# Kernel tuning notes

Hardware: AMD Instinct MI355X
Metric: run time of the kernel (lower is better)

## Reference

```python
import jax, jax.numpy as jnp
import numpy as np

TAU = 2.0        # LIF membrane time constant
VTH = 1.0        # firing threshold
ALPHA = 4.0      # surrogate sigmoid sharpness
BN_EPS = 1e-5

@jax.custom_vjp
def heaviside_surrogate(x):
    # Forward: hard threshold. Backward: sigmoid surrogate gradient (alpha=4).
    return (x >= 0.0).astype(x.dtype)

def _hs_fwd(x):
    return heaviside_surrogate(x), x

def _hs_bwd(x, g):
    s = jax.nn.sigmoid(ALPHA * x)
    return (g * ALPHA * s * (1.0 - s),)

heaviside_surrogate.defvjp(_hs_fwd, _hs_bwd)


def setup_inputs() -> dict:
    key = jax.random.key(0)
    k1, k2 = jax.random.split(key)
    B, Cin, T, Cout = 64, 512, 1024, 256
    x = jax.random.normal(k1, (B, Cin, T), dtype=jnp.float32)
    W = jax.random.normal(k2, (Cout, Cin), dtype=jnp.float32) * (1.0 / np.sqrt(Cin))
    gamma = jnp.ones((Cout,), dtype=jnp.float32)
    beta = jnp.zeros((Cout,), dtype=jnp.float32)
    run_mean = jnp.zeros((Cout,), dtype=jnp.float32)
    run_var = jnp.ones((Cout,), dtype=jnp.float32)
    return {"x": x, "W": W, "gamma": gamma, "beta": beta,
            "run_mean": run_mean, "run_var": run_var}


def reference(x, W, gamma, beta, run_mean, run_var):
    # Dropout is identity in eval mode.
    # conv1d, kernel_size=1, no bias -> pointwise GEMM over channels: [B,Cin,T] -> [B,Cout,T]
    y = jnp.einsum('bct,oc->bot', x, W)
    # BatchNorm1d (inference, running stats), per-channel affine
    inv = jax.lax.rsqrt(run_var + BN_EPS)
    y = (y - run_mean[None, :, None]) * (inv * gamma)[None, :, None] + beta[None, :, None]
    # LIF recurrence over the time dim (last axis), hard reset to 0, detach_reset.
    yt = jnp.transpose(y, (2, 0, 1))  # [T, B, Cout]

    def step(v, x_t):
        v = v + (x_t - v) / TAU              # decay_input charge
        s = heaviside_surrogate(v - VTH)     # spike via surrogate threshold
        v = v * (1.0 - jax.lax.stop_gradient(s))  # hard reset (detached)
        return v, s

    v0 = jnp.zeros(yt.shape[1:], dtype=yt.dtype)
    _, spikes = jax.lax.scan(step, v0, yt)   # spikes: [T, B, Cout]
    # out.mean(dim=-1) == spike rate over time
    return spikes.mean(axis=0)               # [B, Cout]
```

## Files before the change

### kernel.cpp

```cpp
#include <hip/hip_runtime.h>
#include <math.h>

typedef _Float16 f16;
typedef __attribute__((ext_vector_type(8)))  _Float16 f16v8;
typedef __attribute__((ext_vector_type(4)))  __fp16   h16v4;
typedef __attribute__((ext_vector_type(16))) float    f32x16;
typedef __attribute__((ext_vector_type(4)))  float    f32x4;

namespace {
constexpr int kB = 64, kCin = 512, kT = 1024, kCout = 256;
constexpr size_t kYBytes     = (size_t)kB * kT * kCout * 4;
constexpr size_t kWfragBytes = (size_t)32 * 8 * 2 * 64 * 16;
constexpr size_t kSBytes     = kCout * 4;
constexpr size_t kWsNeed     = kYBytes + kWfragBytes + kSBytes;
}

__global__ void wsplit16_kernel(const float* __restrict__ W, const float* __restrict__ gamma,
                                const float* __restrict__ rvar,
                                f16* __restrict__ wfrag, float* __restrict__ sarr) {
    const int kc = blockIdx.x, osub = blockIdx.y, p = blockIdx.z;
    const int lane = threadIdx.x;
    const int o  = osub * 32 + (lane & 31);
    const int kb = kc * 16 + (lane >> 5) * 8;
    f16v8 frag;
#pragma unroll
    for (int j = 0; j < 8; ++j) {
        const float w = 32.0f * W[o * kCin + kb + j];
        const f16 h = (f16)w;
        const float r = w - (float)h;
        const f16 l = (f16)(r * 2048.0f);
        frag[j] = p ? l : h;
    }
    *reinterpret_cast<f16v8*>(wfrag + ((size_t)((kc * 8 + osub) * 2 + p) * 64 + lane) * 8) = frag;
    if (kc == 0 && osub == 0 && p == 0) {
#pragma unroll
        for (int j = 0; j < 4; ++j) {
            const int oo = j * 64 + lane;
            sarr[oo] = (float)((double)gamma[oo] / sqrt((double)rvar[oo] + 1e-5));
        }
    }
}

__global__ __launch_bounds__(512, 2)
void gemm_f16_kernel(const float* __restrict__ x, const f16* __restrict__ wfrag,
                     const float* __restrict__ sarr, const float* __restrict__ rmean,
                     const float* __restrict__ beta, float* __restrict__ yt) {
    __shared__ unsigned int Bd[4][128 * 20];

    const int tid  = threadIdx.x;
    const int lane = tid & 63;
    const int wave = tid >> 6;
    const int n = lane & 31, q = lane >> 5;

    const int bid  = blockIdx.x;
    const int rest = bid >> 3;
    const int b    = (bid & 7) + 8 * (rest >> 3);
    const int tg0  = (rest & 7) * 128;
    const int osg  = wave;
    const float* __restrict__ xb = x + ((size_t)b << 19);
    const f16v8* __restrict__ wf = reinterpret_cast<const f16v8*>(wfrag);

    const int st_t = tid & 127;
    const int kpp  = tid >> 7;
    const int st_sw = (st_t >> 3) & 3;
    const int wr_base = 20 * st_t + 2 * (kpp & 1);
    const int s0 = ((0 + (kpp >> 1)) ^ st_sw) * 4;
    const int s1 = ((2 + (kpp >> 1)) ^ st_sw) * 4;

    f32x16 accA[4] = {};
    f32x16 accB[4] = {};
    f16v8  af[2][2];
    float  xq[4][4];

    auto loadX = [&](int kc, float (&xd)[4]) {
        const float* px = xb + (size_t)(kc * 16 + 4 * kpp) * kT + tg0 + st_t;
#pragma unroll
        for (int r = 0; r < 4; ++r) xd[r] = px[(size_t)r * kT];
    };
    auto loadA = [&](int kc, f16v8 (&ad)[2]) {
#pragma unroll
        for (int pp = 0; pp < 2; ++pp)
            ad[pp] = wf[(size_t)((kc * 8 + osg) * 2 + pp) * 64 + lane];
    };
    auto stage = [&](int buf, const float (&xd)[4]) {
        auto h01 = __builtin_amdgcn_cvt_pkrtz(xd[0], xd[1]);
        auto h23 = __builtin_amdgcn_cvt_pkrtz(xd[2], xd[3]);
        auto l01 = __builtin_amdgcn_cvt_pkrtz((xd[0] - (float)h01[0]) * 2048.0f,
                                              (xd[1] - (float)h01[1]) * 2048.0f);
        auto l23 = __builtin_amdgcn_cvt_pkrtz((xd[2] - (float)h23[0]) * 2048.0f,
                                              (xd[3] - (float)h23[1]) * 2048.0f);
        h16v4 hv, lv;
        hv[0] = h01[0]; hv[1] = h01[1]; hv[2] = h23[0]; hv[3] = h23[1];
        lv[0] = l01[0]; lv[1] = l01[1]; lv[2] = l23[0]; lv[3] = l23[1];
        *reinterpret_cast<h16v4*>(&Bd[buf][wr_base + s0]) = hv;
        *reinterpret_cast<h16v4*>(&Bd[buf][wr_base + s1]) = lv;
    };
    auto domfma = [&](int buf, const f16v8 (&ad)[2]) {
        __builtin_amdgcn_s_setprio(1);
#pragma unroll
        for (int s = 0; s < 4; ++s) {
            const int t = s * 32 + n;
            const int sw = (t >> 3) & 3;
            const f16v8 bh = *reinterpret_cast<const f16v8*>(&Bd[buf][20 * t + 4 * ((0 + q) ^ sw)]);
            const f16v8 bl = *reinterpret_cast<const f16v8*>(&Bd[buf][20 * t + 4 * ((2 + q) ^ sw)]);
            accA[s] = __builtin_amdgcn_mfma_f32_32x32x16_f16(ad[0], bh, accA[s], 0, 0, 0);
            accB[s] = __builtin_amdgcn_mfma_f32_32x32x16_f16(ad[0], bl, accB[s], 0, 0, 0);
            accB[s] = __builtin_amdgcn_mfma_f32_32x32x16_f16(ad[1], bh, accB[s], 0, 0, 0);
        }
        __builtin_amdgcn_s_setprio(0);
    };

    loadX(0, xq[0]); loadX(1, xq[1]); loadX(2, xq[2]); loadX(3, xq[3]);
    loadA(0, af[0]);
    stage(0, xq[0]);
    stage(1, xq[1]);
    asm volatile("s_waitcnt lgkmcnt(0)\n\ts_barrier" ::: "memory");

    for (int kc4 = 0; kc4 < 8; ++kc4) {
#pragma unroll
        for (int u = 0; u < 4; ++u) {
            const int kc = kc4 * 4 + u;
            if (kc < 31) loadA(kc + 1, af[(u + 1) & 1]);
            if (kc < 30) stage((u + 2) & 3, xq[(u + 2) & 3]);
            if (kc < 28) loadX(kc + 4, xq[u]);
            domfma(u, af[u & 1]);
            if (u & 1)
                asm volatile("s_waitcnt lgkmcnt(0)\n\ts_barrier" ::: "memory");
        }
    }

#pragma unroll
    for (int s = 0; s < 4; ++s) {
        const f32x16 v = accA[s] + accB[s] * 4.8828125e-4f;
        const size_t t = (size_t)tg0 + s * 32 + n;
#pragma unroll
        for (int g = 0; g < 4; ++g) {
            const int og = osg * 32 + g * 8 + q * 4;
            const f32x4 sv = *reinterpret_cast<const f32x4*>(sarr + og);
            const f32x4 mv = *reinterpret_cast<const f32x4*>(rmean + og);
            const f32x4 bv = *reinterpret_cast<const f32x4*>(beta + og);
#pragma unroll
            for (int r2 = 0; r2 < 4; ++r2) {
                const int o = og + r2;
                const float val = (v[4 * g + r2] * 0.03125f - mv[r2]) * sv[r2] + bv[r2];
                yt[(((size_t)b << 8) + (size_t)o) * 1024 + t] = val;
            }
        }
    }
}

__global__ __launch_bounds__(64)
void lif_kernel(const float* __restrict__ yt, float* __restrict__ out) {
    const int b = blockIdx.x >> 2;
    const int o = ((blockIdx.x & 3) << 6) + threadIdx.x;
    const f32x4* __restrict__ row =
        reinterpret_cast<const f32x4*>(yt) + (((size_t)b << 8) + (size_t)o) * 256;
    float v = 0.f;
    int cnt = 0;
    f32x4 qb[32];
#pragma unroll
    for (int u = 0; u < 32; ++u) qb[u] = row[u];
    for (int g = 0; g < 7; ++g) {
#pragma unroll
        for (int u = 0; u < 32; ++u) {
            const f32x4 cv = qb[u];
            qb[u] = row[g * 32 + u + 32];
#pragma unroll
            for (int e = 0; e < 4; ++e) {
                v = v + (cv[e] - v) * 0.5f;
                if (v - 1.0f >= 0.0f) { ++cnt; v = 0.f; }
            }
        }
    }
#pragma unroll
    for (int u = 0; u < 32; ++u) {
        const f32x4 cv = qb[u];
#pragma unroll
        for (int e = 0; e < 4; ++e) {
            v = v + (cv[e] - v) * 0.5f;
            if (v - 1.0f >= 0.0f) { ++cnt; v = 0.f; }
        }
    }
    out[((size_t)b << 8) + o] = (float)cnt * (1.0f / 1024.0f);
}

namespace fb {
constexpr int kOTile = 32, kTTile = 128, kCc = 64;
constexpr int kNtt = kT / kTTile, kNcc = kCin / kCc, kYPad = 132;
}

__global__ void wt_transpose_kernel(const float* __restrict__ W, float* __restrict__ Wt) {
    int idx = blockIdx.x * 256 + threadIdx.x;
    int c = idx >> 8, o = idx & 255;
    Wt[idx] = W[o * kCin + c];
}

__global__ __launch_bounds__(256, 2)
void snn_fused_kernel(const float* __restrict__ x, const float* __restrict__ Wt,
                      const float* __restrict__ gamma, const float* __restrict__ beta,
                      const float* __restrict__ rmean, const float* __restrict__ rvar,
                      float* __restrict__ out) {
    using namespace fb;
    __shared__ float xs[kCc][kTTile];
    __shared__ float ws[kCc][kOTile];
    __shared__ float ytile[kOTile][kYPad];
    __shared__ float sarr[kOTile], barr[kOTile], marr[kOTile], vstate[kOTile];
    __shared__ int scnt[kOTile];
    const int tid = threadIdx.x, tx = tid & 31, ty = tid >> 5;
    const int b = blockIdx.y, o_blk = blockIdx.x * kOTile;
    if (tid < kOTile) {
        const int o = o_blk + tid;
        const double dinv = 1.0 / sqrt((double)rvar[o] + 1e-5);
        sarr[tid] = (float)(dinv * (double)gamma[o]);
        barr[tid] = beta[o]; marr[tid] = rmean[o];
        vstate[tid] = 0.0f; scnt[tid] = 0;
    }
    __syncthreads();
    const float* xb = x + (size_t)b * kCin * kT;
    for (int tt = 0; tt < kNtt; ++tt) {
        float acc[4][4];
#pragma unroll
        for (int i = 0; i < 4; ++i)
#pragma unroll
            for (int j = 0; j < 4; ++j) acc[i][j] = 0.0f;
        const int t0 = tt * kTTile;
        for (int cc = 0; cc < kNcc; ++cc) {
#pragma unroll
            for (int k = 0; k < 8; ++k) {
                const int f = tid + 256 * k;
                const int c = f >> 5, tq = f & 31;
                *reinterpret_cast<float4*>(&xs[c][tq * 4]) = *reinterpret_cast<const float4*>(
                    xb + (size_t)(cc * kCc + c) * kT + t0 + tq * 4);
            }
#pragma unroll
            for (int k = 0; k < 2; ++k) {
                const int f = tid + 256 * k;
                const int c = f >> 3, oq = f & 7;
                *reinterpret_cast<float4*>(&ws[c][oq * 4]) = *reinterpret_cast<const float4*>(
                    Wt + (size_t)(cc * kCc + c) * kCout + o_blk + oq * 4);
            }
            __syncthreads();
#pragma unroll 8
            for (int c = 0; c < kCc; ++c) {
                const float4 xv = *reinterpret_cast<const float4*>(&xs[c][tx * 4]);
                const float4 wv = *reinterpret_cast<const float4*>(&ws[c][ty * 4]);
                const float xf[4] = {xv.x, xv.y, xv.z, xv.w};
                const float wf4[4] = {wv.x, wv.y, wv.z, wv.w};
#pragma unroll
                for (int i = 0; i < 4; ++i)
#pragma unroll
                    for (int j = 0; j < 4; ++j) acc[i][j] += wf4[i] * xf[j];
            }
            __syncthreads();
        }
#pragma unroll
        for (int i = 0; i < 4; ++i) {
            const int o = ty * 4 + i;
            const float s = sarr[o], bb2 = barr[o], m = marr[o];
#pragma unroll
            for (int j = 0; j < 4; ++j) ytile[o][tx * 4 + j] = (acc[i][j] - m) * s + bb2;
        }
        __syncthreads();
        if (tid < kOTile) {
            float vv = vstate[tid];
            int cnt = 0;
#pragma unroll 4
            for (int t = 0; t < kTTile; ++t) {
                const float yv = ytile[tid][t];
                vv = vv + (yv - vv) * 0.5f;
                if (vv - 1.0f >= 0.0f) { cnt++; vv = 0.0f; }
            }
            vstate[tid] = vv; scnt[tid] += cnt;
        }
        __syncthreads();
    }
    if (tid < kOTile) out[b * kCout + o_blk + tid] = (float)scnt[tid] * (1.0f / 1024.0f);
}

extern "C" void kernel_launch(void* const* d_in, const int* in_sizes, int n_in,
                              void* d_out, int out_size, void* d_ws, size_t ws_size,
                              hipStream_t stream) {
    const float* x     = (const float*)d_in[0];
    const float* W     = (const float*)d_in[1];
    const float* gamma = (const float*)d_in[2];
    const float* beta  = (const float*)d_in[3];
    const float* rmean = (const float*)d_in[4];
    const float* rvar  = (const float*)d_in[5];
    float* out = (float*)d_out;

    if (ws_size >= kWsNeed) {
        float* yt    = (float*)d_ws;
        f16*   wfrag = (f16*)((char*)d_ws + kYBytes);
        float* sarr  = (float*)((char*)d_ws + kYBytes + kWfragBytes);
        wsplit16_kernel<<<dim3(32, 8, 2), 64, 0, stream>>>(W, gamma, rvar, wfrag, sarr);
        gemm_f16_kernel<<<dim3(512), 512, 0, stream>>>(x, wfrag, sarr, rmean, beta, yt);
        lif_kernel<<<256, 64, 0, stream>>>(yt, out);
    } else {
        float* Wt = (float*)d_ws;
        wt_transpose_kernel<<<(kCin * kCout) / 256, 256, 0, stream>>>(W, Wt);
        snn_fused_kernel<<<dim3(kCout / fb::kOTile, kB), 256, 0, stream>>>(
            x, Wt, gamma, beta, rmean, rvar, out);
    }
}
```

Baseline: 236.5 us.

## Fuse LIF scan into GEMM via per-batch last-block atomic counter

Drops the separate LIF kernel launch. Each GEMM block bumps a per-batch completion counter, and the eighth block to finish for a batch runs the LIF scan over that batch's 256 channels with 256 threads. This removes a kernel launch and lets LIF work overlap with GEMM blocks still running. The trade-off is that LIF work is concentrated in a few tail blocks, each with only 256 active threads and a smaller prefetch buffer. A counter reset is added in the weight-split kernel.

```diff
diff --git a/kernel.cpp b/kernel.cpp
--- a/kernel.cpp
+++ b/kernel.cpp
@@ -12,12 +12,14 @@
 constexpr size_t kYBytes     = (size_t)kB * kT * kCout * 4;
 constexpr size_t kWfragBytes = (size_t)32 * 8 * 2 * 64 * 16;
 constexpr size_t kSBytes     = kCout * 4;
-constexpr size_t kWsNeed     = kYBytes + kWfragBytes + kSBytes;
+constexpr size_t kDoneBytes  = kB * 4;
+constexpr size_t kWsNeed     = kYBytes + kWfragBytes + kSBytes + kDoneBytes;
 }
 
 __global__ void wsplit16_kernel(const float* __restrict__ W, const float* __restrict__ gamma,
                                 const float* __restrict__ rvar,
-                                f16* __restrict__ wfrag, float* __restrict__ sarr) {
+                                f16* __restrict__ wfrag, float* __restrict__ sarr,
+                                unsigned int* __restrict__ done) {
     const int kc = blockIdx.x, osub = blockIdx.y, p = blockIdx.z;
     const int lane = threadIdx.x;
     const int o  = osub * 32 + (lane & 31);
@@ -38,14 +40,17 @@
             const int oo = j * 64 + lane;
             sarr[oo] = (float)((double)gamma[oo] / sqrt((double)rvar[oo] + 1e-5));
         }
+        done[lane] = 0u;
     }
 }
 
 __global__ __launch_bounds__(512, 2)
 void gemm_f16_kernel(const float* __restrict__ x, const f16* __restrict__ wfrag,
                      const float* __restrict__ sarr, const float* __restrict__ rmean,
-                     const float* __restrict__ beta, float* __restrict__ yt) {
+                     const float* __restrict__ beta, float* __restrict__ yt,
+                     float* __restrict__ out, unsigned int* __restrict__ done) {
     __shared__ unsigned int Bd[4][128 * 20];
+    __shared__ unsigned int oldv_sh;
 
     const int tid  = threadIdx.x;
     const int lane = tid & 63;
@@ -147,41 +152,45 @@
             }
         }
     }
-}
-
-__global__ __launch_bounds__(64)
-void lif_kernel(const float* __restrict__ yt, float* __restrict__ out) {
-    const int b = blockIdx.x >> 2;
-    const int o = ((blockIdx.x & 3) << 6) + threadIdx.x;
-    const f32x4* __restrict__ row =
-        reinterpret_cast<const f32x4*>(yt) + (((size_t)b << 8) + (size_t)o) * 256;
-    float v = 0.f;
-    int cnt = 0;
-    f32x4 qb[32];
-#pragma unroll
-    for (int u = 0; u < 32; ++u) qb[u] = row[u];
-    for (int g = 0; g < 7; ++g) {
-#pragma unroll
-        for (int u = 0; u < 32; ++u) {
-            const f32x4 cv = qb[u];
-            qb[u] = row[g * 32 + u + 32];
-#pragma unroll
-            for (int e = 0; e < 4; ++e) {
-                v = v + (cv[e] - v) * 0.5f;
-                if (v - 1.0f >= 0.0f) { ++cnt; v = 0.f; }
-            }
-        }
-    }
-#pragma unroll
-    for (int u = 0; u < 32; ++u) {
-        const f32x4 cv = qb[u];
-#pragma unroll
-        for (int e = 0; e < 4; ++e) {
-            v = v + (cv[e] - v) * 0.5f;
-            if (v - 1.0f >= 0.0f) { ++cnt; v = 0.f; }
-        }
-    }
-    out[((size_t)b << 8) + o] = (float)cnt * (1.0f / 1024.0f);
+
+    __threadfence();
+    if (tid == 0) oldv_sh = atomicAdd(&done[b], 1u);
+    __syncthreads();
+    if (oldv_sh == 7u) {
+        __threadfence();
+        if (tid < 256) {
+            const int o = tid;
+            const f32x4* __restrict__ row =
+                reinterpret_cast<const f32x4*>(yt) + (((size_t)b << 8) + (size_t)o) * 256;
+            float v = 0.f;
+            int cnt = 0;
+            f32x4 qb[16];
+#pragma unroll
+            for (int u2 = 0; u2 < 16; ++u2) qb[u2] = row[u2];
+            for (int jj = 0; jj < 15; ++jj) {
+#pragma unroll
+                for (int u2 = 0; u2 < 16; ++u2) {
+                    const f32x4 cv = qb[u2];
+                    qb[u2] = row[jj * 16 + u2 + 16];
+#pragma unroll
+                    for (int e = 0; e < 4; ++e) {
+                        v = v + (cv[e] - v) * 0.5f;
+                        if (v - 1.0f >= 0.0f) { ++cnt; v = 0.f; }
+                    }
+                }
+            }
+#pragma unroll
+            for (int u2 = 0; u2 < 16; ++u2) {
+                const f32x4 cv = qb[u2];
+#pragma unroll
+                for (int e = 0; e < 4; ++e) {
+                    v = v + (cv[e] - v) * 0.5f;
+                    if (v - 1.0f >= 0.0f) { ++cnt; v = 0.f; }
+                }
+            }
+            out[((size_t)b << 8) + o] = (float)cnt * (1.0f / 1024.0f);
+        }
+    }
 }
 
 namespace fb {
@@ -292,9 +301,9 @@
         float* yt    = (float*)d_ws;
         f16*   wfrag = (f16*)((char*)d_ws + kYBytes);
         float* sarr  = (float*)((char*)d_ws + kYBytes + kWfragBytes);
-        wsplit16_kernel<<<dim3(32, 8, 2), 64, 0, stream>>>(W, gamma, rvar, wfrag, sarr);
-        gemm_f16_kernel<<<dim3(512), 512, 0, stream>>>(x, wfrag, sarr, rmean, beta, yt);
-        lif_kernel<<<256, 64, 0, stream>>>(yt, out);
+        unsigned int* done = (unsigned int*)((char*)d_ws + kYBytes + kWfragBytes + kSBytes);
+        wsplit16_kernel<<<dim3(32, 8, 2), 64, 0, stream>>>(W, gamma, rvar, wfrag, sarr, done);
+        gemm_f16_kernel<<<dim3(512), 512, 0, stream>>>(x, wfrag, sarr, rmean, beta, yt, out, done);
     } else {
         float* Wt = (float*)d_ws;
         wt_transpose_kernel<<<(kCin * kCout) / 256, 256, 0, stream>>>(W, Wt);
```

Result: slower. 420.4 us (+77.8%).
